# Optimization experiments

Hardware: AMD Instinct MI355X
Metric: run time of the kernel (lower is better)

## Reference

```python
import jax, jax.numpy as jnp
import numpy as np

B, S, D = 4, 2048, 1024
H, E = 8, 128  # num_head, num_dim (per-head)

def setup_inputs() -> dict:
    key = jax.random.key(0)
    ks = jax.random.split(key, 8)
    scale_in = 1.0 / np.sqrt(D)
    return {
        "q": jax.random.normal(ks[0], (B, S, D), dtype=jnp.float32),
        "k": jax.random.normal(ks[1], (B, S, D), dtype=jnp.float32),
        "v": jax.random.normal(ks[2], (B, S, D), dtype=jnp.float32),
        "Wq": jax.random.normal(ks[3], (H, D, E), dtype=jnp.float32) * scale_in,
        "Wk": jax.random.normal(ks[4], (H, D, E), dtype=jnp.float32) * scale_in,
        "Wv": jax.random.normal(ks[5], (H, D, E), dtype=jnp.float32) * scale_in,
        "Wo": jax.random.normal(ks[6], (H * E, D), dtype=jnp.float32) * (1.0 / np.sqrt(H * E)),
        "bo": jnp.zeros((D,), dtype=jnp.float32),
    }

def reference(q, k, v, Wq, Wk, Wv, Wo, bo):
    dk = jnp.asarray(E, q.dtype) ** 0.5
    # per-head projections, all heads batched: [B,H,S,E]
    qh = jnp.einsum("bsd,hde->bhse", q, Wq)
    kh = jnp.einsum("bsd,hde->bhse", k, Wk)
    vh = jnp.einsum("bsd,hde->bhse", v, Wv)
    scores = jnp.einsum("bhse,bhte->bhst", qh / dk, kh)  # [B,H,S,S]
    attn = jax.nn.softmax(scores, axis=-1)
    zh = jnp.einsum("bhst,bhte->bhse", attn, vh)  # [B,H,S,E]
    # concat heads along feature dim (head order preserved): [B,S,H*E]
    z = jnp.transpose(zh, (0, 2, 1, 3)).reshape(B, S, H * E)
    return z @ Wo + bo
```

## Files before the change

kernel.cpp:

```cpp
#include <hip/hip_runtime.h>

#define B_ 4
#define S_ 2048
#define D_ 1024
#define H_ 8
#define E_ 128

typedef __bf16 bf16_t;
typedef __bf16 bf16x4 __attribute__((ext_vector_type(4)));
typedef __bf16 bf16x8 __attribute__((ext_vector_type(8)));
typedef float f32x4 __attribute__((ext_vector_type(4)));

#define MFMA16(a, b, c) __builtin_amdgcn_mfma_f32_16x16x32_bf16(a, b, c, 0, 0, 0)

#define LDP_ 72

__device__ __forceinline__ void load_lds16(const bf16_t* g, bf16_t* l) {
    __builtin_amdgcn_global_load_lds(
        (const __attribute__((address_space(1))) unsigned int*)g,
        (__attribute__((address_space(3))) unsigned int*)l,
        16, 0, 0);
}

__device__ __forceinline__ f32x4 zero4() {
    f32x4 z = {0.f, 0.f, 0.f, 0.f};
    return z;
}

__global__ __launch_bounds__(64) void detect_dtype(const unsigned int* __restrict__ q,
                                                   int* __restrict__ flag) {
    int lane = threadIdx.x;
    int cnt = 0;
    for (int i = lane; i < 4096; i += 64) {
        unsigned e = (q[i] >> 7) & 0xFFu;
        cnt += (e >= 110u && e <= 141u) ? 1 : 0;
    }
#pragma unroll
    for (int d = 32; d; d >>= 1) cnt += __shfl_down(cnt, d);
    if (lane == 0) *flag = (cnt > 2048) ? 1 : 0;
}

__global__ __launch_bounds__(256) void convert_bf16(const void* __restrict__ p0,
                                                    const void* __restrict__ p1,
                                                    const void* __restrict__ p2,
                                                    bf16_t* __restrict__ out,
                                                    const int* __restrict__ flagp) {
    const size_t QSZ = (size_t)B_ * H_ * S_ * E_;
    int z = blockIdx.z;
    const void* in = (z == 0) ? p0 : (z == 1) ? p1 : p2;
    bf16_t* o = out + (size_t)z * QSZ;
    int isb = *flagp;
    size_t i = ((size_t)blockIdx.x * 256 + threadIdx.x) * 8;
    if (isb) {
        *(bf16x8*)(o + i) = *(const bf16x8*)((const bf16_t*)in + i);
    } else {
        const float* p = (const float*)in + i;
        f32x4 lo = *(const f32x4*)p;
        f32x4 hi = *(const f32x4*)(p + 4);
        bf16x8 v;
#pragma unroll
        for (int j = 0; j < 4; j++) { v[j] = (bf16_t)lo[j]; v[4 + j] = (bf16_t)hi[j]; }
        *(bf16x8*)(o + i) = v;
    }
}

__global__ __launch_bounds__(256) void transpose_any(const void* __restrict__ p0,
                                                     const void* __restrict__ p1,
                                                     const void* __restrict__ p2,
                                                     bf16_t* __restrict__ out,
                                                     int R, int C,
                                                     const int* __restrict__ flagp) {
    __shared__ bf16_t tile[32][33];
    int isb = *flagp;
    int bz = blockIdx.z;
    int sel = bz >> 3, sub = bz & 7;
    const void* in = (sel == 0) ? p0 : (sel == 1) ? p1 : p2;
    const bf16_t* inb16 = (const bf16_t*)in + (size_t)sub * R * C;
    const float*  inb32 = (const float*)in + (size_t)sub * R * C;
    bf16_t* outb = out + (size_t)bz * R * C;
    int tx = threadIdx.x & 31, ty = threadIdx.x >> 5;
    int r0 = blockIdx.y * 32, c0 = blockIdx.x * 32;
#pragma unroll
    for (int i = 0; i < 4; i++) {
        size_t idx = (size_t)(r0 + ty + i * 8) * C + c0 + tx;
        tile[ty + i * 8][tx] = isb ? inb16[idx] : (bf16_t)inb32[idx];
    }
    __syncthreads();
#pragma unroll
    for (int i = 0; i < 4; i++)
        outb[(size_t)(c0 + ty + i * 8) * R + r0 + tx] = tile[tx][ty + i * 8];
}

__global__ __launch_bounds__(256) void proj_gemm(const bf16_t* __restrict__ Abase,
                                                 int useZ,
                                                 const bf16_t* __restrict__ WtBase,
                                                 bf16_t* __restrict__ OutBase,
                                                 float qscale, int z0) {
    __shared__ __align__(16) bf16_t Alds[128 * 64];
    __shared__ __align__(16) bf16_t Blds[128 * 64];
    const size_t WSZ = (size_t)H_ * E_ * D_;
    const size_t QSZ = (size_t)B_ * H_ * S_ * E_;
    int z = z0 + blockIdx.z;
    const bf16_t* A = Abase + (useZ ? (size_t)z * QSZ : 0);
    const bf16_t* Bt = WtBase + (size_t)z * WSZ + (size_t)blockIdx.y * E_ * D_;
    bf16_t* Out = OutBase + (size_t)z * QSZ;
    int vmode = (z == 2);
    float oscale = (z == 0) ? qscale : 1.0f;

    int m0 = blockIdx.x * 128;
    int h = blockIdx.y;
    int t = threadIdx.x;
    int w = t >> 6, lane = t & 63;
    int quad = lane >> 4, ln = lane & 15;
    int wm = (w >> 1) * 64, wn = (w & 1) * 64;

    f32x4 acc[4][4];
#pragma unroll
    for (int i = 0; i < 4; i++)
#pragma unroll
        for (int j = 0; j < 4; j++) acc[i][j] = zero4();

    for (int k0 = 0; k0 < D_; k0 += 64) {
#pragma unroll
        for (int j = 0; j < 4; j++) {
            int base = j * 256 + w * 64;
            int G = base + lane;
            int r = G >> 3, sl = G & 7;
            int c = sl ^ (r & 7);
            load_lds16(A + (size_t)(m0 + r) * D_ + k0 + c * 8, Alds + (size_t)base * 8);
            load_lds16(Bt + (size_t)r * D_ + k0 + c * 8, Blds + (size_t)base * 8);
        }
        asm volatile("s_waitcnt vmcnt(0)" ::: "memory");
        __syncthreads();

        const bf16_t* Xsrc = vmode ? Blds : Alds;
        const bf16_t* Ysrc = vmode ? Alds : Blds;
#pragma unroll
        for (int ks = 0; ks < 2; ks++) {
            bf16x8 xf[4], yf[4];
#pragma unroll
            for (int mt = 0; mt < 4; mt++) {
                int row = wm + mt * 16 + ln;
                xf[mt] = *(const bf16x8*)(Xsrc + (size_t)row * 64 +
                                          (((ks << 2) + quad) ^ (row & 7)) * 8);
            }
#pragma unroll
            for (int nt = 0; nt < 4; nt++) {
                int row = wn + nt * 16 + ln;
                yf[nt] = *(const bf16x8*)(Ysrc + (size_t)row * 64 +
                                          (((ks << 2) + quad) ^ (row & 7)) * 8);
            }
#pragma unroll
            for (int mt = 0; mt < 4; mt++)
#pragma unroll
                for (int nt = 0; nt < 4; nt++)
                    acc[mt][nt] = MFMA16(xf[mt], yf[nt], acc[mt][nt]);
        }
        __syncthreads();
    }

#pragma unroll
    for (int mt = 0; mt < 4; mt++) {
#pragma unroll
        for (int nt = 0; nt < 4; nt++) {
#pragma unroll
            for (int r = 0; r < 4; r++) {
                int M = wm + mt * 16 + quad * 4 + r;
                int N = wn + nt * 16 + ln;
                float v = acc[mt][nt][r] * oscale;
                size_t idx;
                if (vmode == 0) {
                    int g = m0 + M;
                    int b = g >> 11, s = g & 2047;
                    idx = ((size_t)((b * H_ + h) * S_ + s)) * E_ + N;
                } else {
                    int g = m0 + N;
                    int b = g >> 11, s = g & 2047;
                    idx = ((size_t)((b * H_ + h) * E_ + M)) * S_ + s;
                }
                Out[idx] = (bf16_t)v;
            }
        }
    }
}

__global__ __launch_bounds__(256, 2) void flash_attn(const bf16_t* __restrict__ Qh,
                                                     const bf16_t* __restrict__ Kh,
                                                     const bf16_t* __restrict__ Vt,
                                                     bf16_t* __restrict__ Z) {
    __shared__ __align__(16) bf16_t Klds[64 * 128];
    __shared__ __align__(16) bf16_t Vlds[128 * 64];
    __shared__ __align__(16) bf16_t Plds[4 * 32 * LDP_];
    int bh = blockIdx.y;
    int qt = blockIdx.x;
    const bf16_t* Qbh = Qh + (size_t)bh * S_ * E_;
    const bf16_t* Kbh = Kh + (size_t)bh * S_ * E_;
    const bf16_t* Vbh = Vt + (size_t)bh * E_ * S_;
    int t = threadIdx.x, w = t >> 6, lane = t & 63;
    int quad = lane >> 4, ln = lane & 15;
    bf16_t* Pw = Plds + w * 32 * LDP_;

    bf16x8 qf[2][4];
#pragma unroll
    for (int mt = 0; mt < 2; mt++)
#pragma unroll
        for (int ks = 0; ks < 4; ks++)
            qf[mt][ks] = *(const bf16x8*)(Qbh + (size_t)(qt * 128 + w * 32 + mt * 16 + ln) * E_ +
                                          ks * 32 + quad * 8);

    f32x4 oacc[2][8];
#pragma unroll
    for (int mt = 0; mt < 2; mt++)
#pragma unroll
        for (int nt = 0; nt < 8; nt++) oacc[mt][nt] = zero4();
    float rsum[2] = {0.f, 0.f};

    int koff[4], voff[4], ldso[4];
#pragma unroll
    for (int j = 0; j < 4; j++) {
        int base = j * 256 + w * 64;
        int G = base + lane;
        int rK = G >> 4, cK = (G & 15) ^ (rK & 15);
        int rV = G >> 3, cV = (G & 7) ^ (rV & 7);
        koff[j] = rK * E_ + cK * 8;
        voff[j] = rV * S_ + cV * 8;
        ldso[j] = G * 8;
    }

    bf16x8 gK[4], gV[4];
#pragma unroll
    for (int j = 0; j < 4; j++) {
        gK[j] = *(const bf16x8*)(Kbh + koff[j]);
        gV[j] = *(const bf16x8*)(Vbh + voff[j]);
    }

    const int NT = S_ / 64;
    for (int kt = 0; kt < NT; kt++) {
#pragma unroll
        for (int j = 0; j < 4; j++) {
            *(bf16x8*)(Klds + ldso[j]) = gK[j];
            *(bf16x8*)(Vlds + ldso[j]) = gV[j];
        }
        __syncthreads();

        int ktn = (kt + 1 < NT) ? kt + 1 : kt;
#pragma unroll
        for (int j = 0; j < 4; j++) {
            gK[j] = *(const bf16x8*)(Kbh + (size_t)ktn * 64 * E_ + koff[j]);
            gV[j] = *(const bf16x8*)(Vbh + ktn * 64 + voff[j]);
        }
        __builtin_amdgcn_sched_barrier(0);

#pragma unroll
        for (int nt = 0; nt < 4; nt++) {
            f32x4 sacc[2];
            sacc[0] = zero4();
            sacc[1] = zero4();
            __builtin_amdgcn_s_setprio(1);
#pragma unroll
            for (int ks = 0; ks < 4; ks++) {
                int n = nt * 16 + ln;
                bf16x8 kf = *(const bf16x8*)(Klds + (size_t)n * 128 +
                                             (((ks * 4 + quad) ^ ln) & 15) * 8);
#pragma unroll
                for (int mt = 0; mt < 2; mt++) sacc[mt] = MFMA16(kf, qf[mt][ks], sacc[mt]);
            }
            __builtin_amdgcn_s_setprio(0);
#pragma unroll
            for (int mt = 0; mt < 2; mt++) {
                bf16x4 pk;
#pragma unroll
                for (int r = 0; r < 4; r++) {
                    float p = exp2f(sacc[mt][r] - 18.0f);
                    rsum[mt] += p;
                    pk[r] = (bf16_t)p;
                }
                *(bf16x4*)(Pw + (size_t)(mt * 16 + ln) * LDP_ + nt * 16 + quad * 4) = pk;
            }
        }

        asm volatile("s_waitcnt lgkmcnt(0)" ::: "memory");

        __builtin_amdgcn_s_setprio(1);
#pragma unroll
        for (int ks = 0; ks < 2; ks++) {
            bf16x8 pf[2], vf[8];
#pragma unroll
            for (int mt = 0; mt < 2; mt++)
                pf[mt] = *(const bf16x8*)(Pw + (size_t)(mt * 16 + ln) * LDP_ + ks * 32 + quad * 8);
#pragma unroll
            for (int nt = 0; nt < 8; nt++) {
                int n = nt * 16 + ln;
                vf[nt] = *(const bf16x8*)(Vlds + (size_t)n * 64 +
                                          (((ks * 4 + quad) ^ n) & 7) * 8);
            }
#pragma unroll
            for (int mt = 0; mt < 2; mt++)
#pragma unroll
                for (int nt = 0; nt < 8; nt++)
                    oacc[mt][nt] = MFMA16(pf[mt], vf[nt], oacc[mt][nt]);
        }
        __builtin_amdgcn_s_setprio(0);
        __syncthreads();
    }

    float linv[2][4];
#pragma unroll
    for (int mt = 0; mt < 2; mt++) {
        float v = rsum[mt];
        v += __shfl_xor(v, 16);
        v += __shfl_xor(v, 32);
#pragma unroll
        for (int r = 0; r < 4; r++) linv[mt][r] = 1.0f / __shfl(v, quad * 4 + r);
    }

    int b = bh >> 3, h = bh & 7;
#pragma unroll
    for (int mt = 0; mt < 2; mt++) {
#pragma unroll
        for (int nt = 0; nt < 8; nt++) {
#pragma unroll
            for (int r = 0; r < 4; r++) {
                int s = qt * 128 + w * 32 + mt * 16 + quad * 4 + r;
                int col = h * E_ + nt * 16 + ln;
                Z[((size_t)(b * S_ + s)) * (H_ * E_) + col] =
                    (bf16_t)(oacc[mt][nt][r] * linv[mt][r]);
            }
        }
    }
}

__global__ __launch_bounds__(256) void final_gemm(const bf16_t* __restrict__ A,
                                                  const bf16_t* __restrict__ Bt,
                                                  const void* __restrict__ bias,
                                                  void* __restrict__ Out,
                                                  const int* __restrict__ flagp) {
    __shared__ __align__(16) bf16_t Alds[128 * 64];
    __shared__ __align__(16) bf16_t Blds[128 * 64];
    int isb = *flagp;
    int m0 = blockIdx.x * 128;
    int n0 = blockIdx.y * 128;
    int t = threadIdx.x;
    int w = t >> 6, lane = t & 63;
    int quad = lane >> 4, ln = lane & 15;
    int wm = (w >> 1) * 64, wn = (w & 1) * 64;

    f32x4 acc[4][4];
#pragma unroll
    for (int i = 0; i < 4; i++)
#pragma unroll
        for (int j = 0; j < 4; j++) acc[i][j] = zero4();

    for (int k0 = 0; k0 < D_; k0 += 64) {
#pragma unroll
        for (int j = 0; j < 4; j++) {
            int base = j * 256 + w * 64;
            int G = base + lane;
            int r = G >> 3, sl = G & 7;
            int c = sl ^ (r & 7);
            load_lds16(A + (size_t)(m0 + r) * (H_ * E_) + k0 + c * 8, Alds + (size_t)base * 8);
            load_lds16(Bt + (size_t)(n0 + r) * (H_ * E_) + k0 + c * 8, Blds + (size_t)base * 8);
        }
        asm volatile("s_waitcnt vmcnt(0)" ::: "memory");
        __syncthreads();

#pragma unroll
        for (int ks = 0; ks < 2; ks++) {
            bf16x8 af[4], bfr[4];
#pragma unroll
            for (int mt = 0; mt < 4; mt++) {
                int row = wm + mt * 16 + ln;
                af[mt] = *(const bf16x8*)(Alds + (size_t)row * 64 +
                                          (((ks << 2) + quad) ^ (row & 7)) * 8);
            }
#pragma unroll
            for (int nt = 0; nt < 4; nt++) {
                int row = wn + nt * 16 + ln;
                bfr[nt] = *(const bf16x8*)(Blds + (size_t)row * 64 +
                                           (((ks << 2) + quad) ^ (row & 7)) * 8);
            }
#pragma unroll
            for (int mt = 0; mt < 4; mt++)
#pragma unroll
                for (int nt = 0; nt < 4; nt++)
                    acc[mt][nt] = MFMA16(af[mt], bfr[nt], acc[mt][nt]);
        }
        __syncthreads();
    }

#pragma unroll
    for (int mt = 0; mt < 4; mt++) {
#pragma unroll
        for (int nt = 0; nt < 4; nt++) {
#pragma unroll
            for (int r = 0; r < 4; r++) {
                int grow = m0 + wm + mt * 16 + quad * 4 + r;
                int col = n0 + wn + nt * 16 + ln;
                float bv = isb ? (float)((const bf16_t*)bias)[col]
                               : ((const float*)bias)[col];
                float v = acc[mt][nt][r] + bv;
                size_t idx = (size_t)grow * D_ + col;
                if (isb) ((bf16_t*)Out)[idx] = (bf16_t)v;
                else     ((float*)Out)[idx] = v;
            }
        }
    }
}

extern "C" void kernel_launch(void* const* d_in, const int* in_sizes, int n_in,
                              void* d_out, int out_size, void* d_ws, size_t ws_size,
                              hipStream_t stream) {
    const void* q  = d_in[0];
    const void* k  = d_in[1];
    const void* v  = d_in[2];
    const void* Wq = d_in[3];
    const void* Wk = d_in[4];
    const void* Wv = d_in[5];
    const void* Wo = d_in[6];
    const void* bo = d_in[7];

    int* flag = (int*)d_ws;
    bf16_t* arena = (bf16_t*)((char*)d_ws + 256);
    const size_t WSZ = (size_t)H_ * E_ * D_;
    const size_t QSZ = (size_t)B_ * H_ * S_ * E_;
    bf16_t* wqt = arena;
    bf16_t* wot = wqt + 3 * WSZ;

    const size_t bigBytes = 256 + 2 * (4 * WSZ + 6 * QSZ);
    const bool big = (ws_size >= bigBytes);

    dim3 blk(256);
    const float qscale = 0.08838834764831845f * 1.44269504088896340f;

    detect_dtype<<<dim3(1), dim3(64), 0, stream>>>((const unsigned int*)q, flag);
    transpose_any<<<dim3(4, 32, 24), blk, 0, stream>>>(Wq, Wk, Wv, wqt, D_, E_, flag);
    transpose_any<<<dim3(32, 32, 1), blk, 0, stream>>>(Wo, Wo, Wo, wot, H_ * E_, D_, flag);

    if (big) {
        bf16_t* conv0 = wot + WSZ;
        bf16_t* Qh = conv0 + 3 * QSZ;
        bf16_t* Kh = Qh + QSZ;
        bf16_t* Vt = Kh + QSZ;
        bf16_t* Z  = conv0;

        convert_bf16<<<dim3(4096, 1, 3), blk, 0, stream>>>(q, k, v, conv0, flag);
        proj_gemm<<<dim3(64, 8, 3), blk, 0, stream>>>(conv0, 1, wqt, Qh, qscale, 0);
        flash_attn<<<dim3(16, 32), blk, 0, stream>>>(Qh, Kh, Vt, Z);
        final_gemm<<<dim3(64, 8), blk, 0, stream>>>(Z, wot, bo, d_out, flag);
    } else {
        bf16_t* conv = wot + WSZ;
        bf16_t* Qh = conv + QSZ;
        bf16_t* Kh = Qh + QSZ;
        bf16_t* Vt = Kh + QSZ;
        bf16_t* Z  = conv;

        convert_bf16<<<dim3(4096, 1, 1), blk, 0, stream>>>(q, q, q, conv, flag);
        proj_gemm<<<dim3(64, 8, 1), blk, 0, stream>>>(conv, 0, wqt, Qh, qscale, 0);
        convert_bf16<<<dim3(4096, 1, 1), blk, 0, stream>>>(k, k, k, conv, flag);
        proj_gemm<<<dim3(64, 8, 1), blk, 0, stream>>>(conv, 0, wqt, Qh, qscale, 1);
        convert_bf16<<<dim3(4096, 1, 1), blk, 0, stream>>>(v, v, v, conv, flag);
        proj_gemm<<<dim3(64, 8, 1), blk, 0, stream>>>(conv, 0, wqt, Qh, qscale, 2);
        flash_attn<<<dim3(16, 32), blk, 0, stream>>>(Qh, Kh, Vt, Z);
        final_gemm<<<dim3(64, 8), blk, 0, stream>>>(Z, wot, bo, d_out, flag);
    }
}
```

Before: 377.8 us.

## Fuse fp32-to-bf16 input conversion into projection GEMM and load V directly to registers

Removes the separate convert_bf16 pass: proj_gemm now reads fp32 (or bf16) inputs directly, converts in registers, and stores them into swizzled LDS itself. In flash attention, V fragments are loaded straight from global memory into registers instead of being staged through LDS, which frees LDS and drops the V stores. The P buffer pitch also changes. The trade-offs are that the GEMM A-loads now go through VGPRs with full fp32 traffic, repeated across the 8 head blocks, and that the V global reads are per-lane strided rather than coalesced.

```diff
diff --git a/kernel.cpp b/kernel.cpp
--- a/kernel.cpp
+++ b/kernel.cpp
@@ -13,7 +13,7 @@
 
 #define MFMA16(a, b, c) __builtin_amdgcn_mfma_f32_16x16x32_bf16(a, b, c, 0, 0, 0)
 
-#define LDP_ 72
+#define LDP_ 76
 
 __device__ __forceinline__ void load_lds16(const bf16_t* g, bf16_t* l) {
     __builtin_amdgcn_global_load_lds(
@@ -38,30 +38,6 @@
 #pragma unroll
     for (int d = 32; d; d >>= 1) cnt += __shfl_down(cnt, d);
     if (lane == 0) *flag = (cnt > 2048) ? 1 : 0;
-}
-
-__global__ __launch_bounds__(256) void convert_bf16(const void* __restrict__ p0,
-                                                    const void* __restrict__ p1,
-                                                    const void* __restrict__ p2,
-                                                    bf16_t* __restrict__ out,
-                                                    const int* __restrict__ flagp) {
-    const size_t QSZ = (size_t)B_ * H_ * S_ * E_;
-    int z = blockIdx.z;
-    const void* in = (z == 0) ? p0 : (z == 1) ? p1 : p2;
-    bf16_t* o = out + (size_t)z * QSZ;
-    int isb = *flagp;
-    size_t i = ((size_t)blockIdx.x * 256 + threadIdx.x) * 8;
-    if (isb) {
-        *(bf16x8*)(o + i) = *(const bf16x8*)((const bf16_t*)in + i);
-    } else {
-        const float* p = (const float*)in + i;
-        f32x4 lo = *(const f32x4*)p;
-        f32x4 hi = *(const f32x4*)(p + 4);
-        bf16x8 v;
-#pragma unroll
-        for (int j = 0; j < 4; j++) { v[j] = (bf16_t)lo[j]; v[4 + j] = (bf16_t)hi[j]; }
-        *(bf16x8*)(o + i) = v;
-    }
 }
 
 __global__ __launch_bounds__(256) void transpose_any(const void* __restrict__ p0,
@@ -91,19 +67,22 @@
         outb[(size_t)(c0 + ty + i * 8) * R + r0 + tx] = tile[tx][ty + i * 8];
 }
 
-__global__ __launch_bounds__(256) void proj_gemm(const bf16_t* __restrict__ Abase,
-                                                 int useZ,
+__global__ __launch_bounds__(256) void proj_gemm(const void* __restrict__ p0,
+                                                 const void* __restrict__ p1,
+                                                 const void* __restrict__ p2,
                                                  const bf16_t* __restrict__ WtBase,
                                                  bf16_t* __restrict__ OutBase,
-                                                 float qscale, int z0) {
+                                                 float qscale,
+                                                 const int* __restrict__ flagp) {
     __shared__ __align__(16) bf16_t Alds[128 * 64];
     __shared__ __align__(16) bf16_t Blds[128 * 64];
     const size_t WSZ = (size_t)H_ * E_ * D_;
     const size_t QSZ = (size_t)B_ * H_ * S_ * E_;
-    int z = z0 + blockIdx.z;
-    const bf16_t* A = Abase + (useZ ? (size_t)z * QSZ : 0);
+    int z = blockIdx.z;
+    const void* Ain = (z == 0) ? p0 : (z == 1) ? p1 : p2;
     const bf16_t* Bt = WtBase + (size_t)z * WSZ + (size_t)blockIdx.y * E_ * D_;
     bf16_t* Out = OutBase + (size_t)z * QSZ;
+    int isb = *flagp;
     int vmode = (z == 2);
     float oscale = (z == 0) ? qscale : 1.0f;
 
@@ -121,14 +100,32 @@
         for (int j = 0; j < 4; j++) acc[i][j] = zero4();
 
     for (int k0 = 0; k0 < D_; k0 += 64) {
+        bf16x8 areg[4];
 #pragma unroll
         for (int j = 0; j < 4; j++) {
             int base = j * 256 + w * 64;
             int G = base + lane;
             int r = G >> 3, sl = G & 7;
             int c = sl ^ (r & 7);
-            load_lds16(A + (size_t)(m0 + r) * D_ + k0 + c * 8, Alds + (size_t)base * 8);
+            size_t aoff = (size_t)(m0 + r) * D_ + k0 + c * 8;
+            if (isb) {
+                areg[j] = *(const bf16x8*)((const bf16_t*)Ain + aoff);
+            } else {
+                const float* pa = (const float*)Ain + aoff;
+                f32x4 lo = *(const f32x4*)pa;
+                f32x4 hi = *(const f32x4*)(pa + 4);
+                bf16x8 vv;
+#pragma unroll
+                for (int jj = 0; jj < 4; jj++) { vv[jj] = (bf16_t)lo[jj]; vv[4 + jj] = (bf16_t)hi[jj]; }
+                areg[j] = vv;
+            }
             load_lds16(Bt + (size_t)r * D_ + k0 + c * 8, Blds + (size_t)base * 8);
+        }
+#pragma unroll
+        for (int j = 0; j < 4; j++) {
+            int base = j * 256 + w * 64;
+            int G = base + lane;
+            *(bf16x8*)(Alds + (size_t)G * 8) = areg[j];
         }
         asm volatile("s_waitcnt vmcnt(0)" ::: "memory");
         __syncthreads();
@@ -189,7 +186,6 @@
                                                      const bf16_t* __restrict__ Vt,
                                                      bf16_t* __restrict__ Z) {
     __shared__ __align__(16) bf16_t Klds[64 * 128];
-    __shared__ __align__(16) bf16_t Vlds[128 * 64];
     __shared__ __align__(16) bf16_t Plds[4 * 32 * LDP_];
     int bh = blockIdx.y;
     int qt = blockIdx.x;
@@ -215,40 +211,38 @@
         for (int nt = 0; nt < 8; nt++) oacc[mt][nt] = zero4();
     float rsum[2] = {0.f, 0.f};
 
-    int koff[4], voff[4], ldso[4];
+    int koff[4], ldso[4];
 #pragma unroll
     for (int j = 0; j < 4; j++) {
         int base = j * 256 + w * 64;
         int G = base + lane;
         int rK = G >> 4, cK = (G & 15) ^ (rK & 15);
-        int rV = G >> 3, cV = (G & 7) ^ (rV & 7);
         koff[j] = rK * E_ + cK * 8;
-        voff[j] = rV * S_ + cV * 8;
         ldso[j] = G * 8;
     }
-
-    bf16x8 gK[4], gV[4];
-#pragma unroll
-    for (int j = 0; j < 4; j++) {
-        gK[j] = *(const bf16x8*)(Kbh + koff[j]);
-        gV[j] = *(const bf16x8*)(Vbh + voff[j]);
-    }
+    const bf16_t* vb = Vbh + (size_t)ln * S_ + quad * 8;
+
+    bf16x8 gK[4];
+#pragma unroll
+    for (int j = 0; j < 4; j++) gK[j] = *(const bf16x8*)(Kbh + koff[j]);
 
     const int NT = S_ / 64;
     for (int kt = 0; kt < NT; kt++) {
 #pragma unroll
-        for (int j = 0; j < 4; j++) {
-            *(bf16x8*)(Klds + ldso[j]) = gK[j];
-            *(bf16x8*)(Vlds + ldso[j]) = gV[j];
-        }
+        for (int j = 0; j < 4; j++) *(bf16x8*)(Klds + ldso[j]) = gK[j];
         __syncthreads();
 
         int ktn = (kt + 1 < NT) ? kt + 1 : kt;
 #pragma unroll
-        for (int j = 0; j < 4; j++) {
+        for (int j = 0; j < 4; j++)
             gK[j] = *(const bf16x8*)(Kbh + (size_t)ktn * 64 * E_ + koff[j]);
-            gV[j] = *(const bf16x8*)(Vbh + ktn * 64 + voff[j]);
-        }
+
+        bf16x8 vfr[2][8];
+#pragma unroll
+        for (int ks = 0; ks < 2; ks++)
+#pragma unroll
+            for (int nt = 0; nt < 8; nt++)
+                vfr[ks][nt] = *(const bf16x8*)(vb + (size_t)nt * 16 * S_ + kt * 64 + ks * 32);
         __builtin_amdgcn_sched_barrier(0);
 
 #pragma unroll
@@ -284,21 +278,15 @@
         __builtin_amdgcn_s_setprio(1);
 #pragma unroll
         for (int ks = 0; ks < 2; ks++) {
-            bf16x8 pf[2], vf[8];
+            bf16x8 pf[2];
 #pragma unroll
             for (int mt = 0; mt < 2; mt++)
                 pf[mt] = *(const bf16x8*)(Pw + (size_t)(mt * 16 + ln) * LDP_ + ks * 32 + quad * 8);
 #pragma unroll
-            for (int nt = 0; nt < 8; nt++) {
-                int n = nt * 16 + ln;
-                vf[nt] = *(const bf16x8*)(Vlds + (size_t)n * 64 +
-                                          (((ks * 4 + quad) ^ n) & 7) * 8);
-            }
-#pragma unroll
             for (int mt = 0; mt < 2; mt++)
 #pragma unroll
                 for (int nt = 0; nt < 8; nt++)
-                    oacc[mt][nt] = MFMA16(pf[mt], vf[nt], oacc[mt][nt]);
+                    oacc[mt][nt] = MFMA16(pf[mt], vfr[ks][nt], oacc[mt][nt]);
         }
         __builtin_amdgcn_s_setprio(0);
         __syncthreads();
@@ -425,9 +413,10 @@
     const size_t QSZ = (size_t)B_ * H_ * S_ * E_;
     bf16_t* wqt = arena;
     bf16_t* wot = wqt + 3 * WSZ;
-
-    const size_t bigBytes = 256 + 2 * (4 * WSZ + 6 * QSZ);
-    const bool big = (ws_size >= bigBytes);
+    bf16_t* Qh  = wot + WSZ;
+    bf16_t* Kh  = Qh + QSZ;
+    bf16_t* Vt  = Kh + QSZ;
+    bf16_t* Z   = Vt + QSZ;
 
     dim3 blk(256);
     const float qscale = 0.08838834764831845f * 1.44269504088896340f;
@@ -436,31 +425,7 @@
     transpose_any<<<dim3(4, 32, 24), blk, 0, stream>>>(Wq, Wk, Wv, wqt, D_, E_, flag);
     transpose_any<<<dim3(32, 32, 1), blk, 0, stream>>>(Wo, Wo, Wo, wot, H_ * E_, D_, flag);
 
-    if (big) {
-        bf16_t* conv0 = wot + WSZ;
-        bf16_t* Qh = conv0 + 3 * QSZ;
-        bf16_t* Kh = Qh + QSZ;
-        bf16_t* Vt = Kh + QSZ;
-        bf16_t* Z  = conv0;
-
-        convert_bf16<<<dim3(4096, 1, 3), blk, 0, stream>>>(q, k, v, conv0, flag);
-        proj_gemm<<<dim3(64, 8, 3), blk, 0, stream>>>(conv0, 1, wqt, Qh, qscale, 0);
-        flash_attn<<<dim3(16, 32), blk, 0, stream>>>(Qh, Kh, Vt, Z);
-        final_gemm<<<dim3(64, 8), blk, 0, stream>>>(Z, wot, bo, d_out, flag);
-    } else {
-        bf16_t* conv = wot + WSZ;
-        bf16_t* Qh = conv + QSZ;
-        bf16_t* Kh = Qh + QSZ;
-        bf16_t* Vt = Kh + QSZ;
-        bf16_t* Z  = conv;
-
-        convert_bf16<<<dim3(4096, 1, 1), blk, 0, stream>>>(q, q, q, conv, flag);
-        proj_gemm<<<dim3(64, 8, 1), blk, 0, stream>>>(conv, 0, wqt, Qh, qscale, 0);
-        convert_bf16<<<dim3(4096, 1, 1), blk, 0, stream>>>(k, k, k, conv, flag);
-        proj_gemm<<<dim3(64, 8, 1), blk, 0, stream>>>(conv, 0, wqt, Qh, qscale, 1);
-        convert_bf16<<<dim3(4096, 1, 1), blk, 0, stream>>>(v, v, v, conv, flag);
-        proj_gemm<<<dim3(64, 8, 1), blk, 0, stream>>>(conv, 0, wqt, Qh, qscale, 2);
-        flash_attn<<<dim3(16, 32), blk, 0, stream>>>(Qh, Kh, Vt, Z);
-        final_gemm<<<dim3(64, 8), blk, 0, stream>>>(Z, wot, bo, d_out, flag);
-    }
-}
+    proj_gemm<<<dim3(64, 8, 3), blk, 0, stream>>>(q, k, v, wqt, Qh, qscale, flag);
+    flash_attn<<<dim3(16, 32), blk, 0, stream>>>(Qh, Kh, Vt, Z);
+    final_gemm<<<dim3(64, 8), blk, 0, stream>>>(Z, wot, bo, d_out, flag);
+}
```

New measurement: 489.9 us. 1.3x slower.

## Load V fragments directly from global memory instead of staging through LDS

Applied to the files above, without the earlier changes.

Removes the shared-memory V tile and its register prefetch. Each wave now reads its PV-MFMA V fragments straight from global memory at the start of every key tile. This cuts LDS usage and drops the V LDS stores and reads. In exchange, every wave fetches the whole V tile on its own, so global/L2 traffic for V is multiplied by the number of waves. Those loads are also no longer prefetched one tile ahead, leaving their latency exposed. The P-buffer row pitch is also widened from 72 to 76 elements to change the LDS bank mapping, which leaves the 16-byte P fragment reads misaligned on alternate rows.

```diff
diff --git a/kernel.cpp b/kernel.cpp
--- a/kernel.cpp
+++ b/kernel.cpp
@@ -13,7 +13,7 @@
 
 #define MFMA16(a, b, c) __builtin_amdgcn_mfma_f32_16x16x32_bf16(a, b, c, 0, 0, 0)
 
-#define LDP_ 72
+#define LDP_ 76
 
 __device__ __forceinline__ void load_lds16(const bf16_t* g, bf16_t* l) {
     __builtin_amdgcn_global_load_lds(
@@ -189,7 +189,6 @@
                                                      const bf16_t* __restrict__ Vt,
                                                      bf16_t* __restrict__ Z) {
     __shared__ __align__(16) bf16_t Klds[64 * 128];
-    __shared__ __align__(16) bf16_t Vlds[128 * 64];
     __shared__ __align__(16) bf16_t Plds[4 * 32 * LDP_];
     int bh = blockIdx.y;
     int qt = blockIdx.x;
@@ -215,40 +214,38 @@
         for (int nt = 0; nt < 8; nt++) oacc[mt][nt] = zero4();
     float rsum[2] = {0.f, 0.f};
 
-    int koff[4], voff[4], ldso[4];
+    int koff[4], ldso[4];
 #pragma unroll
     for (int j = 0; j < 4; j++) {
         int base = j * 256 + w * 64;
         int G = base + lane;
         int rK = G >> 4, cK = (G & 15) ^ (rK & 15);
-        int rV = G >> 3, cV = (G & 7) ^ (rV & 7);
         koff[j] = rK * E_ + cK * 8;
-        voff[j] = rV * S_ + cV * 8;
         ldso[j] = G * 8;
     }
-
-    bf16x8 gK[4], gV[4];
-#pragma unroll
-    for (int j = 0; j < 4; j++) {
-        gK[j] = *(const bf16x8*)(Kbh + koff[j]);
-        gV[j] = *(const bf16x8*)(Vbh + voff[j]);
-    }
+    const bf16_t* vb = Vbh + (size_t)ln * S_ + quad * 8;
+
+    bf16x8 gK[4];
+#pragma unroll
+    for (int j = 0; j < 4; j++) gK[j] = *(const bf16x8*)(Kbh + koff[j]);
 
     const int NT = S_ / 64;
     for (int kt = 0; kt < NT; kt++) {
 #pragma unroll
-        for (int j = 0; j < 4; j++) {
-            *(bf16x8*)(Klds + ldso[j]) = gK[j];
-            *(bf16x8*)(Vlds + ldso[j]) = gV[j];
-        }
+        for (int j = 0; j < 4; j++) *(bf16x8*)(Klds + ldso[j]) = gK[j];
         __syncthreads();
 
         int ktn = (kt + 1 < NT) ? kt + 1 : kt;
 #pragma unroll
-        for (int j = 0; j < 4; j++) {
+        for (int j = 0; j < 4; j++)
             gK[j] = *(const bf16x8*)(Kbh + (size_t)ktn * 64 * E_ + koff[j]);
-            gV[j] = *(const bf16x8*)(Vbh + ktn * 64 + voff[j]);
-        }
+
+        bf16x8 vfr[2][8];
+#pragma unroll
+        for (int ks = 0; ks < 2; ks++)
+#pragma unroll
+            for (int nt = 0; nt < 8; nt++)
+                vfr[ks][nt] = *(const bf16x8*)(vb + (size_t)nt * 16 * S_ + kt * 64 + ks * 32);
         __builtin_amdgcn_sched_barrier(0);
 
 #pragma unroll
@@ -284,21 +281,15 @@
         __builtin_amdgcn_s_setprio(1);
 #pragma unroll
         for (int ks = 0; ks < 2; ks++) {
-            bf16x8 pf[2], vf[8];
+            bf16x8 pf[2];
 #pragma unroll
             for (int mt = 0; mt < 2; mt++)
                 pf[mt] = *(const bf16x8*)(Pw + (size_t)(mt * 16 + ln) * LDP_ + ks * 32 + quad * 8);
 #pragma unroll
-            for (int nt = 0; nt < 8; nt++) {
-                int n = nt * 16 + ln;
-                vf[nt] = *(const bf16x8*)(Vlds + (size_t)n * 64 +
-                                          (((ks * 4 + quad) ^ n) & 7) * 8);
-            }
-#pragma unroll
             for (int mt = 0; mt < 2; mt++)
 #pragma unroll
                 for (int nt = 0; nt < 8; nt++)
-                    oacc[mt][nt] = MFMA16(pf[mt], vf[nt], oacc[mt][nt]);
+                    oacc[mt][nt] = MFMA16(pf[mt], vfr[ks][nt], oacc[mt][nt]);
         }
         __builtin_amdgcn_s_setprio(0);
         __syncthreads();
```

After: 413.7 us. +9.5%, slower.
